# Kernel optimization log

Measured on AMD Instinct MI355X. Metric: run time of the kernel, lower is better.

The kernel has to match this reference:

```python
import jax, jax.numpy as jnp
import numpy as np

N_NODES = 100000
N_EDGES = 1600000
F_IN = 512
HIDDEN = 64
N_CLASS = 16


def spmm(edge_src, edge_dst, edge_val, dense):
    # sparse [N,N] @ dense [N,D] via gather-scale-scatter
    gathered = dense[edge_src] * edge_val[:, None]          # [E, D]
    return jax.ops.segment_sum(gathered, edge_dst, num_segments=N_NODES)


def setup_inputs() -> dict:
    key = jax.random.key(0)
    ks = jax.random.split(key, 8)
    return {
        "x": jax.random.normal(ks[0], (N_NODES, F_IN), dtype=jnp.float32),
        "edge_src": jax.random.randint(ks[1], (N_EDGES,), 0, N_NODES, dtype=jnp.int32),
        "edge_dst": jax.random.randint(ks[2], (N_EDGES,), 0, N_NODES, dtype=jnp.int32),
        "edge_val": jax.random.uniform(ks[3], (N_EDGES,), dtype=jnp.float32),
        "W1": jax.random.normal(ks[4], (F_IN, HIDDEN), dtype=jnp.float32) * (1.0 / np.sqrt(HIDDEN)),
        "b1": jax.random.normal(ks[5], (HIDDEN,), dtype=jnp.float32) * 0.01,
        "W2": jax.random.normal(ks[6], (HIDDEN, N_CLASS), dtype=jnp.float32) * (1.0 / np.sqrt(N_CLASS)),
        "b2": jax.random.normal(ks[7], (N_CLASS,), dtype=jnp.float32) * 0.01,
    }


def reference(x, edge_src, edge_dst, edge_val, W1, b1, W2, b2):
    # Layer 1: support = x @ W1 ; out = A @ support + b1 ; relu
    h = spmm(edge_src, edge_dst, edge_val, x @ W1) + b1      # [N, 64]
    h = jax.nn.relu(h)
    # dropout with training=False is identity (eval forward)
    # Layer 2
    logits = spmm(edge_src, edge_dst, edge_val, h @ W2) + b2  # [N, C]
    return jax.nn.softmax(logits, axis=1)
```

## Files before the change

kernel.cpp:

```cpp
#include <hip/hip_runtime.h>
#include <hip/hip_bf16.h>

#define N_NODES 100000
#define N_EDGES 1600000
#define F_IN    512
#define HID     64
#define NCLS    16

#define SCAN_NB 98
#define BM      128
#define BK      128
#define PA_EPB  4096
#define PA_NB   ((N_EDGES + PA_EPB - 1) / PA_EPB)

typedef __attribute__((ext_vector_type(8))) short short8;
typedef __attribute__((ext_vector_type(4))) float f32x4;
typedef unsigned int u32;
typedef unsigned short u16;

__device__ inline void gload_lds16(const float* g, float* l) {
    __builtin_amdgcn_global_load_lds(
        (const __attribute__((address_space(1))) u32*)g,
        (__attribute__((address_space(3))) u32*)l, 16, 0, 0);
}

__global__ __launch_bounds__(256) void bhist(const int* __restrict__ edst,
                                             int* __restrict__ bh) {
    __shared__ int hist[SCAN_NB];
    int tid = threadIdx.x;
    int e00 = blockIdx.x * PA_EPB;
    for (int i = tid; i < SCAN_NB; i += 256) hist[i] = 0;
    __syncthreads();
    #pragma unroll
    for (int j = 0; j < PA_EPB / 256; j++) {
        int e = e00 + j * 256 + tid;
        if (e < N_EDGES) atomicAdd(&hist[edst[e] >> 10], 1);
    }
    __syncthreads();
    for (int i = tid; i < SCAN_NB; i += 256)
        bh[i * PA_NB + blockIdx.x] = hist[i];
}

__global__ __launch_bounds__(512) void colscan(int* __restrict__ bh,
                                               int* __restrict__ bsums) {
    __shared__ int sc[512];
    int t = threadIdx.x;
    int b = blockIdx.x;
    int v = (t < PA_NB) ? bh[b * PA_NB + t] : 0;
    sc[t] = v;
    __syncthreads();
    #pragma unroll
    for (int d = 1; d < 512; d <<= 1) {
        int u = (t >= d) ? sc[t - d] : 0;
        __syncthreads();
        sc[t] += u;
        __syncthreads();
    }
    if (t < PA_NB) bh[b * PA_NB + t] = sc[t] - v;
    if (t == 511) bsums[b] = sc[511];
}

__global__ __launch_bounds__(128) void scan_top(const int* __restrict__ bsums,
                                                int* __restrict__ bbase,
                                                int* __restrict__ off) {
    __shared__ int sc[128];
    int t = threadIdx.x;
    int v0 = (t < SCAN_NB) ? bsums[t] : 0;
    sc[t] = v0;
    __syncthreads();
    #pragma unroll
    for (int d = 1; d < 128; d <<= 1) {
        int v = (t >= d) ? sc[t - d] : 0;
        __syncthreads();
        sc[t] += v;
        __syncthreads();
    }
    bbase[t] = sc[t] - v0;
    if (t == 0) off[N_NODES] = N_EDGES;
}

__global__ __launch_bounds__(256) void partA2(const int* __restrict__ esrc,
                                              const int* __restrict__ edst,
                                              const float* __restrict__ eval_,
                                              const int* __restrict__ bh,
                                              const int* __restrict__ bbase,
                                              int2* __restrict__ mid) {
    __shared__ int curs[SCAN_NB];
    int tid = threadIdx.x;
    int blk = blockIdx.x;
    int e00 = blk * PA_EPB;
    for (int i = tid; i < SCAN_NB; i += 256)
        curs[i] = bbase[i] + bh[i * PA_NB + blk];
    __syncthreads();
    #pragma unroll
    for (int j = 0; j < PA_EPB / 256; j++) {
        int e = e00 + j * 256 + tid;
        if (e < N_EDGES) {
            int d = edst[e];
            int b = d >> 10;
            int pos = atomicAdd(&curs[b], 1);
            mid[pos] = make_int2(esrc[e] | ((d & 1023) << 17),
                                 __float_as_int(eval_[e]));
        }
    }
}

__global__ __launch_bounds__(512) void partB2(const int* __restrict__ bbase,
                                              const int* __restrict__ bsums,
                                              const int2* __restrict__ mid,
                                              int2* __restrict__ epk,
                                              int* __restrict__ off) {
    __shared__ int nh[1024];
    __shared__ int sc[512];
    int t = threadIdx.x;
    int b = blockIdx.x;
    int start = bbase[b];
    int cntb  = bsums[b];

    nh[t] = 0; nh[t + 512] = 0;
    __syncthreads();

    for (int i = t; i < cntb; i += 512) {
        u32 ux = (u32)mid[start + i].x;
        atomicAdd(&nh[ux >> 17], 1);
    }
    __syncthreads();

    int c0 = nh[2 * t], c1 = nh[2 * t + 1];
    int s = c0 + c1;
    sc[t] = s;
    __syncthreads();
    #pragma unroll
    for (int d = 1; d < 512; d <<= 1) {
        int u = (t >= d) ? sc[t - d] : 0;
        __syncthreads();
        sc[t] += u;
        __syncthreads();
    }
    int ex = start + sc[t] - s;

    nh[2 * t]     = ex;
    nh[2 * t + 1] = ex + c0;
    int node = (b << 10) + 2 * t;
    if (node < N_NODES)     off[node]     = ex;
    if (node + 1 < N_NODES) off[node + 1] = ex + c0;
    __syncthreads();

    for (int i = t; i < cntb; i += 512) {
        int2 m = mid[start + i];
        u32 ux = (u32)m.x;
        int pos = atomicAdd(&nh[ux >> 17], 1);
        epk[pos] = make_int2((int)(ux & 0x1FFFF), m.y);
    }
}

__device__ inline void split_bf16(float a, unsigned short& hi, unsigned short& lo) {
    unsigned u = __float_as_uint(a);
    hi = (unsigned short)(u >> 16);
    float hif = __uint_as_float(((unsigned)hi) << 16);
    float lof = a - hif;
    lo = (unsigned short)(__float_as_uint(lof) >> 16);
}

__device__ inline void split8(f32x4 a, f32x4 b, short8& hi, short8& lo) {
    #pragma unroll
    for (int i = 0; i < 4; i++) {
        u16 h, l;
        split_bf16(a[i], h, l);
        hi[i] = (short)h; lo[i] = (short)l;
    }
    #pragma unroll
    for (int i = 0; i < 4; i++) {
        u16 h, l;
        split_bf16(b[i], h, l);
        hi[4 + i] = (short)h; lo[4 + i] = (short)l;
    }
}

__global__ __launch_bounds__(256) void prep_w1(const float* __restrict__ W1,
                                               unsigned short* __restrict__ Wg) {
    int idx = blockIdx.x * 256 + threadIdx.x;
    if (idx >= F_IN * HID) return;
    int k = idx >> 6, n = idx & 63;
    unsigned short hi, lo;
    split_bf16(W1[idx], hi, lo);
    int nt = n >> 4, kc = k >> 5;
    int l  = ((k >> 3) & 3) * 16 + (n & 15);
    int j  = k & 7;
    long base = ((((long)nt * 16 + kc) * 2) * 64 + l) * 8 + j;
    Wg[base]       = hi;
    Wg[base + 512] = lo;
}

__global__ __launch_bounds__(256, 2) void gemm1_mfma(const float* __restrict__ x,
                                                     const unsigned short* __restrict__ Wg,
                                                     float* __restrict__ support) {
    __shared__ float tile[BM * BK];

    const int tid  = threadIdx.x;
    const int l    = tid & 63;
    const int w    = tid >> 6;
    const int lr   = l & 15;
    const int lg   = l >> 4;
    const int row0 = blockIdx.x * BM;

    f32x4 acc[2][4] = {};

    for (int kb = 0; kb < F_IN; kb += BK) {
        #pragma unroll
        for (int j = 0; j < 16; j++) {
            int slotbase = j * 256 + w * 64;
            int slot     = slotbase + l;
            int row      = slot >> 5;
            int cl       = (slot & 31) ^ (row & 7);
            int rr       = row0 + row;
            if (rr > N_NODES - 1) rr = N_NODES - 1;
            gload_lds16(x + (long)rr * F_IN + kb + cl * 4, tile + slotbase * 4);
        }
        __syncthreads();

        #pragma unroll
        for (int ks = 0; ks < 4; ks++) {
            int kc = (kb >> 5) + ks;
            short8 ah[2], al[2];
            #pragma unroll
            for (int m = 0; m < 2; m++) {
                int r  = m * 64 + w * 16 + lr;
                int c0 = ks * 8 + lg * 2;
                f32x4 v0 = *(const f32x4*)&tile[r * BK + ((c0 ^ (r & 7)) << 2)];
                f32x4 v1 = *(const f32x4*)&tile[r * BK + (((c0 + 1) ^ (r & 7)) << 2)];
                split8(v0, v1, ah[m], al[m]);
            }
            #pragma unroll
            for (int nt = 0; nt < 4; nt++) {
                long bo = ((((long)nt * 16 + kc) * 2) * 64 + l) * 8;
                short8 bh = *(const short8*)(Wg + bo);
                short8 bl = *(const short8*)(Wg + bo + 512);
                #pragma unroll
                for (int m = 0; m < 2; m++) {
                    acc[m][nt] = __builtin_amdgcn_mfma_f32_16x16x32_bf16(ah[m], bh, acc[m][nt], 0, 0, 0);
                    acc[m][nt] = __builtin_amdgcn_mfma_f32_16x16x32_bf16(ah[m], bl, acc[m][nt], 0, 0, 0);
                    acc[m][nt] = __builtin_amdgcn_mfma_f32_16x16x32_bf16(al[m], bh, acc[m][nt], 0, 0, 0);
                }
            }
        }
        __syncthreads();
    }

    #pragma unroll
    for (int m = 0; m < 2; m++) {
        #pragma unroll
        for (int nt = 0; nt < 4; nt++) {
            #pragma unroll
            for (int r = 0; r < 4; r++) {
                int row = row0 + m * 64 + w * 16 + lg * 4 + r;
                if (row < N_NODES)
                    support[(long)row * HID + nt * 16 + lr] = acc[m][nt][r];
            }
        }
    }
}

__global__ __launch_bounds__(256) void spmm1_fused(const int* __restrict__ off,
                                                   const int2* __restrict__ epk,
                                                   const float* __restrict__ sup,
                                                   const float* __restrict__ b1,
                                                   const float* __restrict__ W2,
                                                   float* __restrict__ sup2) {
    __shared__ float w2s[HID * NCLS];
    __shared__ float hrow[4][HID];
    int tid = threadIdx.x;
    for (int i = tid; i < HID * NCLS; i += 256) w2s[i] = W2[i];
    __syncthreads();

    int lane = tid & 63;
    int w    = tid >> 6;
    int n    = blockIdx.x * 4 + w;

    int e0 = off[n];
    int e1 = off[n + 1];
    float acc = 0.f;
    int e = e0;
    for (; e + 7 < e1; e += 8) {
        int2 p[8];
        float g[8];
        #pragma unroll
        for (int j = 0; j < 8; j++) p[j] = epk[e + j];
        #pragma unroll
        for (int j = 0; j < 8; j++) g[j] = sup[(long)p[j].x * HID + lane];
        #pragma unroll
        for (int j = 0; j < 8; j++) acc += __int_as_float(p[j].y) * g[j];
    }
    for (; e + 3 < e1; e += 4) {
        int2 p0 = epk[e],     p1 = epk[e + 1];
        int2 p2 = epk[e + 2], p3 = epk[e + 3];
        float g0 = sup[(long)p0.x * HID + lane];
        float g1 = sup[(long)p1.x * HID + lane];
        float g2 = sup[(long)p2.x * HID + lane];
        float g3 = sup[(long)p3.x * HID + lane];
        acc += __int_as_float(p0.y) * g0 + __int_as_float(p1.y) * g1
             + __int_as_float(p2.y) * g2 + __int_as_float(p3.y) * g3;
    }
    for (; e < e1; e++) {
        int2 p = epk[e];
        acc += __int_as_float(p.y) * sup[(long)p.x * HID + lane];
    }
    float hv = fmaxf(acc + b1[lane], 0.f);

    hrow[w][lane] = hv;
    asm volatile("s_waitcnt lgkmcnt(0)" ::: "memory");
    __builtin_amdgcn_sched_barrier(0);

    int c = lane & 15, q = lane >> 4;
    float part = 0.f;
    #pragma unroll
    for (int k0 = 0; k0 < 16; k0++) {
        int k = q * 16 + k0;
        part += hrow[w][k] * w2s[k * NCLS + c];
    }
    part += __shfl_xor(part, 16);
    part += __shfl_xor(part, 32);
    if (lane < 16) sup2[(long)n * NCLS + c] = part;
}

__global__ __launch_bounds__(256) void spmm2_softmax(const int* __restrict__ off,
                                                     const int2* __restrict__ epk,
                                                     const float* __restrict__ sup2,
                                                     const float* __restrict__ b2,
                                                     float* __restrict__ out) {
    int tid = threadIdx.x;
    int n   = blockIdx.x * 16 + (tid >> 4);
    int c   = tid & 15;
    if (n >= N_NODES) return;

    int e0 = off[n];
    int e1 = off[n + 1];
    float acc = 0.f;
    int e = e0;
    for (; e + 7 < e1; e += 8) {
        int2 p[8];
        float g[8];
        #pragma unroll
        for (int j = 0; j < 8; j++) p[j] = epk[e + j];
        #pragma unroll
        for (int j = 0; j < 8; j++) g[j] = sup2[(long)p[j].x * NCLS + c];
        #pragma unroll
        for (int j = 0; j < 8; j++) acc += __int_as_float(p[j].y) * g[j];
    }
    for (; e + 3 < e1; e += 4) {
        int2 p0 = epk[e],     p1 = epk[e + 1];
        int2 p2 = epk[e + 2], p3 = epk[e + 3];
        float g0 = sup2[(long)p0.x * NCLS + c];
        float g1 = sup2[(long)p1.x * NCLS + c];
        float g2 = sup2[(long)p2.x * NCLS + c];
        float g3 = sup2[(long)p3.x * NCLS + c];
        acc += __int_as_float(p0.y) * g0 + __int_as_float(p1.y) * g1
             + __int_as_float(p2.y) * g2 + __int_as_float(p3.y) * g3;
    }
    for (; e < e1; e++) {
        int2 p = epk[e];
        acc += __int_as_float(p.y) * sup2[(long)p.x * NCLS + c];
    }

    float lg = acc + b2[c];
    float m = lg;
    #pragma unroll
    for (int mask = 1; mask < 16; mask <<= 1)
        m = fmaxf(m, __shfl_xor(m, mask, 16));
    float p = expf(lg - m);
    float s = p;
    #pragma unroll
    for (int mask = 1; mask < 16; mask <<= 1)
        s += __shfl_xor(s, mask, 16);
    out[(long)n * NCLS + c] = p / s;
}

extern "C" void kernel_launch(void* const* d_in, const int* in_sizes, int n_in,
                              void* d_out, int out_size, void* d_ws, size_t ws_size,
                              hipStream_t stream) {
    const float* x     = (const float*)d_in[0];
    const int*   esrc  = (const int*)  d_in[1];
    const int*   edst  = (const int*)  d_in[2];
    const float* eval_ = (const float*)d_in[3];
    const float* W1    = (const float*)d_in[4];
    const float* b1    = (const float*)d_in[5];
    const float* W2    = (const float*)d_in[6];
    const float* b2    = (const float*)d_in[7];
    float* out = (float*)d_out;

    float* sup1  = (float*)d_ws;
    float* sup2  = sup1 + (long)N_NODES * HID;
    int2*  epk   = (int2*)(sup2 + (long)N_NODES * NCLS);
    int*   off   = (int*)(epk + N_EDGES);
    int*   bsums = off + 100004;
    int*   bbase = bsums + 128;
    int*   bh    = bbase + 128;
    unsigned short* Wg = (unsigned short*)(bh + 38320);
    int2*  mid   = (int2*)(Wg + 65536);

    bhist  <<<PA_NB,   256, 0, stream>>>(edst, bh);
    colscan<<<SCAN_NB, 512, 0, stream>>>(bh, bsums);
    scan_top<<<1,      128, 0, stream>>>(bsums, bbase, off);
    partA2 <<<PA_NB,   256, 0, stream>>>(esrc, edst, eval_, bh, bbase, mid);
    partB2 <<<SCAN_NB, 512, 0, stream>>>(bbase, bsums, mid, epk, off);

    prep_w1<<<(F_IN * HID + 255) / 256, 256, 0, stream>>>(W1, Wg);
    gemm1_mfma<<<(N_NODES + BM - 1) / BM, 256, 0, stream>>>(x, Wg, sup1);
    spmm1_fused<<<N_NODES / 4, 256, 0, stream>>>(off, epk, sup1, b1, W2, sup2);

    spmm2_softmax<<<(N_NODES + 15) / 16, 256, 0, stream>>>(off, epk, sup2, b2, out);
}
```

Measured before the change: 228.7 us.

## Double-buffer GEMM1 LDS tiles and pad SpMM edge loops to eight-wide batches

The x@W1 MFMA GEMM now uses two 64-wide K tiles in LDS. It issues the async global-to-LDS load for the next tile before computing on the current one, so loads overlap with MFMA work and one barrier per iteration is dropped. Both SpMM kernels replace their 8/4/1 remainder loops with a single 8-wide loop. Out-of-range slots there re-read the first edge and are zero-weighted, which keeps more gathers in flight for low-degree nodes at the cost of redundant loads. LDS use stays the same, but smaller K tiles mean more iterations and barriers.

```diff
diff --git a/kernel.cpp b/kernel.cpp
--- a/kernel.cpp
+++ b/kernel.cpp
@@ -9,7 +9,6 @@
 
 #define SCAN_NB 98
 #define BM      128
-#define BK      128
 #define PA_EPB  4096
 #define PA_NB   ((N_EDGES + PA_EPB - 1) / PA_EPB)
 
@@ -195,7 +194,7 @@
 __global__ __launch_bounds__(256, 2) void gemm1_mfma(const float* __restrict__ x,
                                                      const unsigned short* __restrict__ Wg,
                                                      float* __restrict__ support) {
-    __shared__ float tile[BM * BK];
+    __shared__ float tile[2][BM * 64];
 
     const int tid  = threadIdx.x;
     const int l    = tid & 63;
@@ -206,29 +205,35 @@
 
     f32x4 acc[2][4] = {};
 
-    for (int kb = 0; kb < F_IN; kb += BK) {
-        #pragma unroll
-        for (int j = 0; j < 16; j++) {
+    auto stage = [&](int buf, int kb) {
+        #pragma unroll
+        for (int j = 0; j < 8; j++) {
             int slotbase = j * 256 + w * 64;
             int slot     = slotbase + l;
-            int row      = slot >> 5;
-            int cl       = (slot & 31) ^ (row & 7);
+            int row      = slot >> 4;
+            int cl       = (slot & 15) ^ (row & 7);
             int rr       = row0 + row;
             if (rr > N_NODES - 1) rr = N_NODES - 1;
-            gload_lds16(x + (long)rr * F_IN + kb + cl * 4, tile + slotbase * 4);
+            gload_lds16(x + (long)rr * F_IN + kb + cl * 4, &tile[buf][slotbase * 4]);
         }
-        __syncthreads();
-
-        #pragma unroll
-        for (int ks = 0; ks < 4; ks++) {
-            int kc = (kb >> 5) + ks;
+    };
+
+    stage(0, 0);
+    int cur = 0;
+    for (int t = 0; t < 8; t++) {
+        __syncthreads();
+        if (t < 7) stage(cur ^ 1, (t + 1) * 64);
+
+        #pragma unroll
+        for (int ks = 0; ks < 2; ks++) {
+            int kc = t * 2 + ks;
             short8 ah[2], al[2];
             #pragma unroll
             for (int m = 0; m < 2; m++) {
                 int r  = m * 64 + w * 16 + lr;
                 int c0 = ks * 8 + lg * 2;
-                f32x4 v0 = *(const f32x4*)&tile[r * BK + ((c0 ^ (r & 7)) << 2)];
-                f32x4 v1 = *(const f32x4*)&tile[r * BK + (((c0 + 1) ^ (r & 7)) << 2)];
+                f32x4 v0 = *(const f32x4*)&tile[cur][r * 64 + ((c0 ^ (r & 7)) << 2)];
+                f32x4 v1 = *(const f32x4*)&tile[cur][r * 64 + (((c0 + 1) ^ (r & 7)) << 2)];
                 split8(v0, v1, ah[m], al[m]);
             }
             #pragma unroll
@@ -244,7 +249,7 @@
                 }
             }
         }
-        __syncthreads();
+        cur ^= 1;
     }
 
     #pragma unroll
@@ -280,30 +285,19 @@
     int e0 = off[n];
     int e1 = off[n + 1];
     float acc = 0.f;
-    int e = e0;
-    for (; e + 7 < e1; e += 8) {
+    for (int e = e0; e < e1; e += 8) {
+        int rem = e1 - e;
         int2 p[8];
         float g[8];
         #pragma unroll
-        for (int j = 0; j < 8; j++) p[j] = epk[e + j];
-        #pragma unroll
-        for (int j = 0; j < 8; j++) g[j] = sup[(long)p[j].x * HID + lane];
-        #pragma unroll
-        for (int j = 0; j < 8; j++) acc += __int_as_float(p[j].y) * g[j];
-    }
-    for (; e + 3 < e1; e += 4) {
-        int2 p0 = epk[e],     p1 = epk[e + 1];
-        int2 p2 = epk[e + 2], p3 = epk[e + 3];
-        float g0 = sup[(long)p0.x * HID + lane];
-        float g1 = sup[(long)p1.x * HID + lane];
-        float g2 = sup[(long)p2.x * HID + lane];
-        float g3 = sup[(long)p3.x * HID + lane];
-        acc += __int_as_float(p0.y) * g0 + __int_as_float(p1.y) * g1
-             + __int_as_float(p2.y) * g2 + __int_as_float(p3.y) * g3;
-    }
-    for (; e < e1; e++) {
-        int2 p = epk[e];
-        acc += __int_as_float(p.y) * sup[(long)p.x * HID + lane];
+        for (int j = 0; j < 8; j++)
+            p[j] = epk[e + ((j < rem) ? j : 0)];
+        #pragma unroll
+        for (int j = 0; j < 8; j++)
+            g[j] = sup[(long)p[j].x * HID + lane];
+        #pragma unroll
+        for (int j = 0; j < 8; j++)
+            acc += ((j < rem) ? __int_as_float(p[j].y) : 0.f) * g[j];
     }
     float hv = fmaxf(acc + b1[lane], 0.f);
 
@@ -336,30 +330,19 @@
     int e0 = off[n];
     int e1 = off[n + 1];
     float acc = 0.f;
-    int e = e0;
-    for (; e + 7 < e1; e += 8) {
+    for (int e = e0; e < e1; e += 8) {
+        int rem = e1 - e;
         int2 p[8];
         float g[8];
         #pragma unroll
-        for (int j = 0; j < 8; j++) p[j] = epk[e + j];
-        #pragma unroll
-        for (int j = 0; j < 8; j++) g[j] = sup2[(long)p[j].x * NCLS + c];
-        #pragma unroll
-        for (int j = 0; j < 8; j++) acc += __int_as_float(p[j].y) * g[j];
-    }
-    for (; e + 3 < e1; e += 4) {
-        int2 p0 = epk[e],     p1 = epk[e + 1];
-        int2 p2 = epk[e + 2], p3 = epk[e + 3];
-        float g0 = sup2[(long)p0.x * NCLS + c];
-        float g1 = sup2[(long)p1.x * NCLS + c];
-        float g2 = sup2[(long)p2.x * NCLS + c];
-        float g3 = sup2[(long)p3.x * NCLS + c];
-        acc += __int_as_float(p0.y) * g0 + __int_as_float(p1.y) * g1
-             + __int_as_float(p2.y) * g2 + __int_as_float(p3.y) * g3;
-    }
-    for (; e < e1; e++) {
-        int2 p = epk[e];
-        acc += __int_as_float(p.y) * sup2[(long)p.x * NCLS + c];
+        for (int j = 0; j < 8; j++)
+            p[j] = epk[e + ((j < rem) ? j : 0)];
+        #pragma unroll
+        for (int j = 0; j < 8; j++)
+            g[j] = sup2[(long)p[j].x * NCLS + c];
+        #pragma unroll
+        for (int j = 0; j < 8; j++)
+            acc += ((j < rem) ? __int_as_float(p[j].y) : 0.f) * g[j];
     }
 
     float lg = acc + b2[c];
```

After: 236.7 us. 3.5% more time.
